# Optimization experiments

Hardware: AMD Instinct MI355X
Metric: run time of the kernel (lower is better)

Reference implementation:

```python
import jax, jax.numpy as jnp
import numpy as np

D = 32        # feature/embedding dim (init arg d)
T = 2049      # tokens: N+1 with N=2048
N_LAYER = 2
N_HEAD = 2
VAR = 0.02


def setup_inputs() -> dict:
    key = jax.random.key(0)
    k1, k2 = jax.random.split(key)
    Z = jax.random.normal(k1, (D, T), dtype=jnp.float32)
    # allparam ~ N(0, var); channel 0 = V, 1 = B, 2 = C
    allparam = VAR * jax.random.normal(k2, (N_LAYER, N_HEAD, 3, D, D), dtype=jnp.float32)
    return {"Z": Z, "allparam": allparam}


def _gb_activation(U, W):
    # Attn[i, j] = prod_k heaviside(U[k, i] * W[k, j], 0)
    # == 1 iff U[:, i] and W[:, j] agree in (strict) sign for every coordinate.
    # Original code detaches + round-trips through numpy -> no gradient: stop_gradient.
    gate = jnp.heaviside(U[:, :, None] * W[:, None, :], jnp.float32(0.0))  # (d, T, T)
    return jax.lax.stop_gradient(jnp.prod(gate, axis=0))  # (T, T)


def _attention(V, B, C, Z):
    t = Z.shape[1]
    attn = _gb_activation(B @ Z, C @ Z)            # (T, T)
    key = V @ Z                                    # (d, T)
    M = jnp.eye(t, dtype=Z.dtype).at[t - 1, t - 1].set(0.0)  # mask query token
    return jnp.einsum('ik,kl,lj->ij', key, M, attn)  # (d, T)


def reference(Z, allparam):
    n_layer, n_head = allparam.shape[0], allparam.shape[1]
    for i in range(n_layer):
        Zi = Z
        residues = jnp.zeros_like(Zi)
        for j in range(n_head):
            Vij = allparam[i, j, 0]
            Bij = allparam[i, j, 1]
            Cij = allparam[i, j, 2]
            residues = residues + _attention(Vij, Bij, Cij, Zi)
        Z = Zi + residues
    return Z
```

## Files before the change

kernel.cpp:

```cpp
#include <hip/hip_runtime.h>

#define D 32
#define T 2049
#define NH 2
#define NBLK 257
#define PAD 33

typedef unsigned long long u64;


__device__ __forceinline__ void sig_from_lds(
    const float (*Bs)[32][PAD], const float (*Cs)[32][PAD],
    const float* Zcol,
    int tid, int t,
    u64* __restrict__ sigU, u64* __restrict__ sigW)
{
    const int k = tid & 31;
    #pragma unroll
    for (int h = 0; h < NH; ++h) {
        float u = 0.f, w = 0.f;
        #pragma unroll
        for (int d = 0; d < 32; ++d) {
            float z = Zcol[d];
            u += Bs[h][k][d] * z;
            w += Cs[h][k][d] * z;
        }
        u64 pu = __ballot(u > 0.0f);
        u64 zu = __ballot(u == 0.0f);
        u64 pw = __ballot(w > 0.0f);
        u64 zw = __ballot(w == 0.0f);
        const int wid = tid & 63;
        if ((wid == 0 || wid == 32) && t < T) {
            const int sh = (wid == 0) ? 0 : 32;
            u64 su = (unsigned int)(pu >> sh);
            if ((unsigned int)(zu >> sh)) su |= (1ull << 32);
            u64 sw = (unsigned int)(pw >> sh);
            if ((unsigned int)(zw >> sh)) sw |= (1ull << 32);
            sigU[h * T + t] = su;
            sigW[h * T + t] = sw;
        }
    }
}

__global__ __launch_bounds__(256) void sig0_kernel(
    const float* __restrict__ Z, const float* __restrict__ allparam,
    u64* __restrict__ sigU, u64* __restrict__ sigW)
{
    const int tid = threadIdx.x, b = blockIdx.x;
    __shared__ float Bs[NH][32][PAD];
    __shared__ float Cs[NH][32][PAD];
    __shared__ float Zs[8][32];

    #pragma unroll
    for (int h = 0; h < NH; ++h) {
        const float* Bp = allparam + (h * 3 + 1) * 1024;
        const float* Cp = allparam + (h * 3 + 2) * 1024;
        #pragma unroll
        for (int i = 0; i < 4; ++i) {
            int idx = tid + 256 * i;
            Bs[h][idx >> 5][idx & 31] = Bp[idx];
            Cs[h][idx >> 5][idx & 31] = Cp[idx];
        }
    }
    {
        int d = tid >> 3, c = tid & 7;
        int t = b * 8 + c; if (t >= T) t = T - 1;
        Zs[c][d] = Z[d * T + t];
    }
    __syncthreads();

    const int c = tid >> 5;
    sig_from_lds(Bs, Cs, Zs[c], tid, b * 8 + c, sigU, sigW);
}

__device__ __forceinline__ void attn_scan(
    const float* __restrict__ Zin, const float* __restrict__ pbase,
    const u64* __restrict__ sigU, const u64* __restrict__ sigW,
    int j0, int j1, int lane, int k, float& acc0, float& acc1)
{
    #pragma unroll
    for (int h = 0; h < NH; ++h) {
        u64 wv0 = (j0 < T) ? sigW[h * T + j0] : ~0ull;
        u64 wv1 = (j1 < T) ? sigW[h * T + j1] : ~0ull;
        const bool s0 = (wv0 >> 32) != 0;
        const bool s1 = (wv1 >> 32) != 0;
        if (s0 && s1) continue;
        const float* V = pbase + h * 3 * 1024;
        const u64* su = sigU + h * T;
        for (int it0 = 0; it0 < 32; it0 += 8) {
            u64 sv[8];
            #pragma unroll
            for (int q = 0; q < 8; ++q)
                sv[q] = su[(it0 + q) * 64 + lane];
            #pragma unroll
            for (int q = 0; q < 8; ++q) {
                u64 m0 = __ballot(!s0 && sv[q] == wv0);
                u64 m1 = __ballot(!s1 && sv[q] == wv1);
                while (m0) {
                    const int bb = __builtin_ctzll(m0); m0 &= m0 - 1;
                    const int lm = (it0 + q) * 64 + bb;
                    float kv = 0.f;
                    #pragma unroll
                    for (int d = 0; d < 32; ++d)
                        kv += V[k * 32 + d] * Zin[d * T + lm];
                    acc0 += kv;
                }
                while (m1) {
                    const int bb = __builtin_ctzll(m1); m1 &= m1 - 1;
                    const int lm = (it0 + q) * 64 + bb;
                    float kv = 0.f;
                    #pragma unroll
                    for (int d = 0; d < 32; ++d)
                        kv += V[k * 32 + d] * Zin[d * T + lm];
                    acc1 += kv;
                }
            }
        }
    }
}

__global__ __launch_bounds__(256) void attn_sig_kernel(
    const float* __restrict__ Zin, const float* __restrict__ allparam,
    const u64* __restrict__ sig0U, const u64* __restrict__ sig0W,
    u64* __restrict__ sig1U, u64* __restrict__ sig1W,
    float* __restrict__ Zout)
{
    const int tid = threadIdx.x, b = blockIdx.x;
    const int w = tid >> 6, lane = tid & 63, k = lane & 31, half = lane >> 5;
    const int j0 = b * 8 + w * 2, j1 = j0 + 1;

    __shared__ float Bs[NH][32][PAD];
    __shared__ float Cs[NH][32][PAD];
    __shared__ float Zs[8][32];

    const float* p1 = allparam + NH * 3 * 1024;
    #pragma unroll
    for (int h = 0; h < NH; ++h) {
        const float* Bp = p1 + (h * 3 + 1) * 1024;
        const float* Cp = p1 + (h * 3 + 2) * 1024;
        #pragma unroll
        for (int i = 0; i < 4; ++i) {
            int idx = tid + 256 * i;
            Bs[h][idx >> 5][idx & 31] = Bp[idx];
            Cs[h][idx >> 5][idx & 31] = Cp[idx];
        }
    }

    float acc0 = 0.f, acc1 = 0.f;
    attn_scan(Zin, allparam, sig0U, sig0W, j0, j1, lane, k, acc0, acc1);

    const int jc   = half ? j1 : j0;
    const float ac = half ? acc1 : acc0;
    float r = 0.f;
    if (jc < T) {
        r = Zin[k * T + jc] + ac;
        Zout[k * T + jc] = r;
    }
    Zs[w * 2 + half][k] = r;
    __syncthreads();

    const int c = tid >> 5;
    sig_from_lds(Bs, Cs, Zs[c], tid, b * 8 + c, sig1U, sig1W);
}

__global__ __launch_bounds__(256) void attn_kernel(
    const float* __restrict__ Zin, const float* __restrict__ allparam,
    const u64* __restrict__ sigU, const u64* __restrict__ sigW,
    float* __restrict__ Zout)
{
    const int tid = threadIdx.x, b = blockIdx.x;
    const int w = tid >> 6, lane = tid & 63, k = lane & 31, half = lane >> 5;
    const int j0 = b * 8 + w * 2, j1 = j0 + 1;
    const float* p1 = allparam + NH * 3 * 1024;

    float acc0 = 0.f, acc1 = 0.f;
    attn_scan(Zin, p1, sigU, sigW, j0, j1, lane, k, acc0, acc1);

    const int jc   = half ? j1 : j0;
    const float ac = half ? acc1 : acc0;
    if (jc < T) Zout[k * T + jc] = Zin[k * T + jc] + ac;
}

extern "C" void kernel_launch(void* const* d_in, const int* in_sizes, int n_in,
                              void* d_out, int out_size, void* d_ws, size_t ws_size,
                              hipStream_t stream) {
    const float* Z        = (const float*)d_in[0];
    const float* allparam = (const float*)d_in[1];
    float* out            = (float*)d_out;

    float* Zmid = (float*)d_ws;
    size_t off = ((size_t)D * T * sizeof(float) + 255) & ~(size_t)255;
    u64* sig0U = (u64*)((char*)d_ws + off);
    u64* sig0W = sig0U + (size_t)NH * T;
    u64* sig1U = sig0W + (size_t)NH * T;
    u64* sig1W = sig1U + (size_t)NH * T;

    sig0_kernel<<<NBLK, 256, 0, stream>>>(Z, allparam, sig0U, sig0W);
    attn_sig_kernel<<<NBLK, 256, 0, stream>>>(Z, allparam, sig0U, sig0W,
                                              sig1U, sig1W, Zmid);
    attn_kernel<<<NBLK, 256, 0, stream>>>(Zmid, allparam, sig1U, sig1W, out);
}
```

Measured before the change: 75.05 us.

## Split key scan across waves with LDS reduction over block query columns

Before, each wave owned two query columns and scanned all 2048 key signatures for them. Now each of the four waves scans one quarter of the keys for all eight query columns in the block. Partial sums go into a shared-memory buffer and are reduced after a barrier. Each wave loads a quarter as many key signatures and keeps them in registers, at the cost of an extra barrier, LDS traffic and eight accumulators per thread. It may also change how matching work is balanced across waves.

```diff
diff --git a/kernel.cpp b/kernel.cpp
--- a/kernel.cpp
+++ b/kernel.cpp
@@ -73,49 +73,52 @@
     sig_from_lds(Bs, Cs, Zs[c], tid, b * 8 + c, sigU, sigW);
 }
 
-__device__ __forceinline__ void attn_scan(
+__device__ __forceinline__ void attn_scan_block(
     const float* __restrict__ Zin, const float* __restrict__ pbase,
     const u64* __restrict__ sigU, const u64* __restrict__ sigW,
-    int j0, int j1, int lane, int k, float& acc0, float& acc1)
-{
-    #pragma unroll
-    for (int h = 0; h < NH; ++h) {
-        u64 wv0 = (j0 < T) ? sigW[h * T + j0] : ~0ull;
-        u64 wv1 = (j1 < T) ? sigW[h * T + j1] : ~0ull;
-        const bool s0 = (wv0 >> 32) != 0;
-        const bool s1 = (wv1 >> 32) != 0;
-        if (s0 && s1) continue;
+    int b, int tid, float (*accs)[8][32])
+{
+    const int w = tid >> 6, lane = tid & 63, k = lane & 31;
+    float acc[8] = {0.f,0.f,0.f,0.f,0.f,0.f,0.f,0.f};
+
+    u64 sv0[8], sv1[8];
+    #pragma unroll
+    for (int q = 0; q < 8; ++q) sv0[q] = sigU[0 * T + w * 512 + q * 64 + lane];
+    #pragma unroll
+    for (int q = 0; q < 8; ++q) sv1[q] = sigU[1 * T + w * 512 + q * 64 + lane];
+
+    #pragma unroll
+    for (int h = 0; h < NH; ++h) {
+        const u64* sv = h ? sv1 : sv0;
         const float* V = pbase + h * 3 * 1024;
-        const u64* su = sigU + h * T;
-        for (int it0 = 0; it0 < 32; it0 += 8) {
-            u64 sv[8];
+        u64 wv[8]; bool alive[8];
+        #pragma unroll
+        for (int c = 0; c < 8; ++c) {
+            int j = b * 8 + c;
+            wv[c] = (j < T) ? sigW[h * T + j] : ~0ull;
+            alive[c] = ((wv[c] >> 32) == 0);
+        }
+        #pragma unroll
+        for (int q = 0; q < 8; ++q) {
             #pragma unroll
-            for (int q = 0; q < 8; ++q)
-                sv[q] = su[(it0 + q) * 64 + lane];
-            #pragma unroll
-            for (int q = 0; q < 8; ++q) {
-                u64 m0 = __ballot(!s0 && sv[q] == wv0);
-                u64 m1 = __ballot(!s1 && sv[q] == wv1);
-                while (m0) {
-                    const int bb = __builtin_ctzll(m0); m0 &= m0 - 1;
-                    const int lm = (it0 + q) * 64 + bb;
+            for (int c = 0; c < 8; ++c) {
+                if (!alive[c]) continue;
+                u64 m = __ballot(sv[q] == wv[c]);
+                while (m) {
+                    const int bb = __builtin_ctzll(m); m &= m - 1;
+                    const int lm = w * 512 + q * 64 + bb;
                     float kv = 0.f;
                     #pragma unroll
                     for (int d = 0; d < 32; ++d)
                         kv += V[k * 32 + d] * Zin[d * T + lm];
-                    acc0 += kv;
-                }
-                while (m1) {
-                    const int bb = __builtin_ctzll(m1); m1 &= m1 - 1;
-                    const int lm = (it0 + q) * 64 + bb;
-                    float kv = 0.f;
-                    #pragma unroll
-                    for (int d = 0; d < 32; ++d)
-                        kv += V[k * 32 + d] * Zin[d * T + lm];
-                    acc1 += kv;
+                    acc[c] += kv;
                 }
             }
         }
+    }
+    if (lane < 32) {
+        #pragma unroll
+        for (int c = 0; c < 8; ++c) accs[w][c][k] = acc[c];
     }
 }
 
@@ -126,12 +129,10 @@
     float* __restrict__ Zout)
 {
     const int tid = threadIdx.x, b = blockIdx.x;
-    const int w = tid >> 6, lane = tid & 63, k = lane & 31, half = lane >> 5;
-    const int j0 = b * 8 + w * 2, j1 = j0 + 1;
-
     __shared__ float Bs[NH][32][PAD];
     __shared__ float Cs[NH][32][PAD];
     __shared__ float Zs[8][32];
+    __shared__ float accs[4][8][32];
 
     const float* p1 = allparam + NH * 3 * 1024;
     #pragma unroll
@@ -146,21 +147,21 @@
         }
     }
 
-    float acc0 = 0.f, acc1 = 0.f;
-    attn_scan(Zin, allparam, sig0U, sig0W, j0, j1, lane, k, acc0, acc1);
-
-    const int jc   = half ? j1 : j0;
-    const float ac = half ? acc1 : acc0;
+    attn_scan_block(Zin, allparam, sig0U, sig0W, b, tid, accs);
+    __syncthreads();
+
+    const int c = tid >> 5, k = tid & 31;
+    const int j = b * 8 + c;
     float r = 0.f;
-    if (jc < T) {
-        r = Zin[k * T + jc] + ac;
-        Zout[k * T + jc] = r;
-    }
-    Zs[w * 2 + half][k] = r;
-    __syncthreads();
-
-    const int c = tid >> 5;
-    sig_from_lds(Bs, Cs, Zs[c], tid, b * 8 + c, sig1U, sig1W);
+    if (j < T) {
+        r = Zin[k * T + j]
+          + accs[0][c][k] + accs[1][c][k] + accs[2][c][k] + accs[3][c][k];
+        Zout[k * T + j] = r;
+    }
+    Zs[c][k] = r;
+    __syncthreads();
+
+    sig_from_lds(Bs, Cs, Zs[c], tid, j, sig1U, sig1W);
 }
 
 __global__ __launch_bounds__(256) void attn_kernel(
@@ -169,16 +170,19 @@
     float* __restrict__ Zout)
 {
     const int tid = threadIdx.x, b = blockIdx.x;
-    const int w = tid >> 6, lane = tid & 63, k = lane & 31, half = lane >> 5;
-    const int j0 = b * 8 + w * 2, j1 = j0 + 1;
+    __shared__ float accs[4][8][32];
     const float* p1 = allparam + NH * 3 * 1024;
 
-    float acc0 = 0.f, acc1 = 0.f;
-    attn_scan(Zin, p1, sigU, sigW, j0, j1, lane, k, acc0, acc1);
-
-    const int jc   = half ? j1 : j0;
-    const float ac = half ? acc1 : acc0;
-    if (jc < T) Zout[k * T + jc] = Zin[k * T + jc] + ac;
+    attn_scan_block(Zin, p1, sigU, sigW, b, tid, accs);
+    __syncthreads();
+
+    const int c = tid >> 5, k = tid & 31;
+    const int j = b * 8 + c;
+    if (j < T) {
+        float r = Zin[k * T + j]
+          + accs[0][c][k] + accs[1][c][k] + accs[2][c][k] + accs[3][c][k];
+        Zout[k * T + j] = r;
+    }
 }
 
 extern "C" void kernel_launch(void* const* d_in, const int* in_sizes, int n_in,
```

After: 86.73 us. +15.6%, slower.
